# Kernel optimization log

Measured on AMD Instinct MI355X. Metric: run time of the kernel, lower is better.

Reference implementation:

```python
import jax, jax.numpy as jnp
import numpy as np

N_NODES = 50000
N_EDGES = 800000


def graph_conv(h, W, b, src, dst, n_nodes):
    # DGL GraphConv with norm='both':
    #   out = D_in^{-1/2} * A^T * (D_out^{-1/2} * h) @ W + b
    ones = jnp.ones((src.shape[0],), dtype=h.dtype)
    deg_out = jax.ops.segment_sum(ones, src, num_segments=n_nodes)
    deg_in = jax.ops.segment_sum(ones, dst, num_segments=n_nodes)
    norm_src = jnp.clip(deg_out, 1.0) ** -0.5  # [N]
    norm_dst = jnp.clip(deg_in, 1.0) ** -0.5   # [N]
    msg = (h * norm_src[:, None])[src]          # [E, F] gather
    agg = jax.ops.segment_sum(msg, dst, num_segments=n_nodes)  # [N, F] scatter
    return (agg * norm_dst[:, None]) @ W + b


def setup_inputs() -> dict:
    key = jax.random.key(0)
    ks = jax.random.split(key, 5)
    h = jax.random.normal(ks[0], (N_NODES, 64), dtype=jnp.float32)
    src = jax.random.randint(ks[1], (N_EDGES,), 0, N_NODES, dtype=jnp.int32)
    dst = jax.random.randint(ks[2], (N_EDGES,), 0, N_NODES, dtype=jnp.int32)
    W1 = jax.random.normal(ks[3], (64, 128), dtype=jnp.float32) * (1.0 / np.sqrt(64))
    b1 = jnp.zeros((128,), dtype=jnp.float32)
    W2 = jax.random.normal(ks[4], (128, 64), dtype=jnp.float32) * (1.0 / np.sqrt(128))
    b2 = jnp.zeros((64,), dtype=jnp.float32)
    return {"h": h, "src": src, "dst": dst, "W1": W1, "b1": b1, "W2": W2, "b2": b2}


def reference(h, src, dst, W1, b1, W2, b2):
    n = h.shape[0]
    h1 = jax.nn.relu(graph_conv(h, W1, b1, src, dst, n))
    out = graph_conv(h1, W2, b2, src, dst, n)
    return out
```

## Files before the change

### kernel.cpp

```cpp
#include <hip/hip_runtime.h>


#define NBMAX 512
#define CAPLOG 12
#define CAP (1 << CAPLOG)
#define NB_BIN 256

typedef __attribute__((ext_vector_type(8))) short bf16x8;
typedef __attribute__((ext_vector_type(4))) float f32x4;

__device__ inline unsigned short f2bf(float f) {
    unsigned int u = __float_as_uint(f);
    unsigned int r = (u + 0x7FFFu + ((u >> 16) & 1u)) >> 16;
    return (unsigned short)r;
}
__device__ inline float bf2f_lo(unsigned int u) { return __uint_as_float(u << 16); }
__device__ inline float bf2f_hi(unsigned int u) { return __uint_as_float(u & 0xFFFF0000u); }

__global__ __launch_bounds__(256) void hist_edges(const int* __restrict__ src,
        const int* __restrict__ dst, int* __restrict__ hist, int n_edges, int nb,
        const float* __restrict__ W1, const float* __restrict__ W2,
        unsigned short* __restrict__ w1t_g, unsigned short* __restrict__ w2t_g) {
    if (blockIdx.x == gridDim.x - 1) {
        for (int i = threadIdx.x; i < 8192; i += 256) {
            int k = i >> 7, nn = i & 127;
            w1t_g[nn * 72 + k] = f2bf(W1[i]);
        }
        for (int i = threadIdx.x; i < 8192; i += 256) {
            int k = i >> 6, nn = i & 63;
            w2t_g[nn * 136 + k] = f2bf(W2[i]);
        }
        return;
    }
    __shared__ int hs[NBMAX], hd[NBMAX];
    for (int i = threadIdx.x; i < nb; i += 256) { hs[i] = 0; hd[i] = 0; }
    __syncthreads();
    int chunk = (n_edges + NB_BIN - 1) / NB_BIN;
    int e0 = blockIdx.x * chunk;
    int e1 = e0 + chunk; if (e1 > n_edges) e1 = n_edges;
    for (int e = e0 + (int)threadIdx.x; e < e1; e += 256) {
        atomicAdd(&hs[src[e] >> 7], 1);
        atomicAdd(&hd[dst[e] >> 7], 1);
    }
    __syncthreads();
    int* rs = hist + (size_t)blockIdx.x * NBMAX;
    int* rd = hist + (size_t)(NB_BIN + blockIdx.x) * NBMAX;
    for (int i = threadIdx.x; i < nb; i += 256) { rs[i] = hs[i]; rd[i] = hd[i]; }
}

__global__ __launch_bounds__(256) void scan_hist(const int* __restrict__ hist,
        int* __restrict__ offs, int* __restrict__ cnt_s, int* __restrict__ cnt_d,
        int nb) {
    __shared__ int wtot[4];
    int j = blockIdx.x;
    int side = j >= nb ? 1 : 0;
    int bucket = j - side * nb;
    const int tid = threadIdx.x;
    size_t idx = (size_t)(side * NB_BIN + tid) * NBMAX + bucket;
    int v = hist[idx];
    int lane = tid & 63, wid = tid >> 6;
    int incl = v;
    #pragma unroll
    for (int d = 1; d < 64; d <<= 1) {
        int t = __shfl_up(incl, d, 64);
        if (lane >= d) incl += t;
    }
    if (lane == 63) wtot[wid] = incl;
    __syncthreads();
    int pre = 0;
    #pragma unroll
    for (int k = 0; k < 3; ++k) if (k < wid) pre += wtot[k];
    int excl = pre + incl - v;
    offs[idx] = excl;
    if (tid == 255) {
        int tot = excl + v;
        if (side) cnt_d[bucket] = tot; else cnt_s[bucket] = tot;
    }
}

__global__ __launch_bounds__(256) void scatter_binned(const int* __restrict__ src,
        const int* __restrict__ dst, const int* __restrict__ offs,
        unsigned char* __restrict__ ss, unsigned int* __restrict__ sd,
        int n_edges, int nb) {
    __shared__ int cs[NBMAX], cd[NBMAX];
    for (int i = threadIdx.x; i < nb; i += 256) {
        cs[i] = offs[(size_t)blockIdx.x * NBMAX + i];
        cd[i] = offs[(size_t)(NB_BIN + blockIdx.x) * NBMAX + i];
    }
    __syncthreads();
    int chunk = (n_edges + NB_BIN - 1) / NB_BIN;
    int e0 = blockIdx.x * chunk;
    int e1 = e0 + chunk; if (e1 > n_edges) e1 = n_edges;
    for (int e = e0 + (int)threadIdx.x; e < e1; e += 256) {
        int s = src[e], d = dst[e];
        int sb = s >> 7, db = d >> 7;
        int ps = atomicAdd(&cs[sb], 1);
        ss[((size_t)sb << CAPLOG) + ps] = (unsigned char)(s & 127);
        int pd = atomicAdd(&cd[db], 1);
        sd[((size_t)db << CAPLOG) + pd] = ((unsigned int)(d & 127) << 25) | (unsigned int)s;
    }
}

__global__ __launch_bounds__(256) void prep(const float* __restrict__ h,
        const unsigned char* __restrict__ ss, const int* __restrict__ cnt_s,
        const unsigned int* __restrict__ sd, const int* __restrict__ cnt_d,
        float* __restrict__ norm_src, unsigned short* __restrict__ xb,
        int2* __restrict__ node_rng, unsigned short* __restrict__ srt,
        float* __restrict__ norm_dst, int n) {
    __shared__ int cnt[128], cur[128];
    __shared__ float nrm[128];
    __shared__ int w0tot;
    const int b = blockIdx.x;
    const int tid = threadIdx.x;

    if (tid < 128) cnt[tid] = 0;
    __syncthreads();
    {
        int used = cnt_s[b];
        const unsigned char* p = ss + ((size_t)b << CAPLOG);
        for (int i = tid; i < used; i += 256) atomicAdd(&cnt[p[i]], 1);
    }
    __syncthreads();
    if (tid < 128) {
        int c = cnt[tid]; if (c < 1) c = 1;
        float s = 1.0f / sqrtf((float)c);
        nrm[tid] = s;
        int node = (b << 7) + tid;
        if (node < n) norm_src[node] = s;
    }
    __syncthreads();
    {
        int base = b << 7;
        for (int t = tid; t < 128 * 16; t += 256) {
            int r = t >> 4, c4 = (t & 15) << 2;
            int node = base + r;
            if (node < n) {
                float s = nrm[r];
                float4 v = *(const float4*)(h + (size_t)node * 64 + c4);
                ushort4 o;
                o.x = f2bf(v.x * s); o.y = f2bf(v.y * s);
                o.z = f2bf(v.z * s); o.w = f2bf(v.w * s);
                *(ushort4*)(xb + (size_t)node * 64 + c4) = o;
            }
        }
    }
    __syncthreads();

    if (tid < 128) cnt[tid] = 0;
    __syncthreads();
    int used = cnt_d[b];
    const unsigned int* p = sd + ((size_t)b << CAPLOG);
    for (int i = tid; i < used; i += 256) atomicAdd(&cnt[p[i] >> 25], 1);
    __syncthreads();
    int lane = tid & 63, wid = tid >> 6;
    int v = (tid < 128) ? cnt[tid] : 0;
    int incl = v;
    #pragma unroll
    for (int d = 1; d < 64; d <<= 1) {
        int t = __shfl_up(incl, d, 64);
        if (lane >= d) incl += t;
    }
    if (tid == 63) w0tot = incl;
    __syncthreads();
    if (tid < 128) {
        int excl = incl - v + (wid == 1 ? w0tot : 0);
        cur[tid] = excl;
        int node = (b << 7) + tid;
        if (node < n) {
            int base = b << CAPLOG;
            node_rng[node] = make_int2(base + excl, base + excl + v);
            int c = v; if (c < 1) c = 1;
            norm_dst[node] = 1.0f / sqrtf((float)c);
        }
    }
    __syncthreads();
    for (int i = tid; i < used; i += 256) {
        unsigned int e = p[i];
        int l = (int)(e >> 25);
        int pos = atomicAdd(&cur[l], 1);
        srt[((size_t)b << CAPLOG) + pos] = (unsigned short)(e & 0xFFFFu);
    }
}

__global__ __launch_bounds__(256) void gather24(const unsigned short* __restrict__ xb,
        const unsigned short* __restrict__ srt, const int2* __restrict__ node_rng,
        const float* __restrict__ nrm, const float* __restrict__ bias,
        void* __restrict__ outp, int write_bf, int n_nodes) {
    int node = blockIdx.x * 4 + (threadIdx.x >> 6);
    if (node >= n_nodes) return;
    int lane = threadIdx.x & 63;
    int g  = lane >> 3;
    int c8 = (lane & 7) * 8;
    int2 rng = node_rng[node];
    int a0 = rng.x, a1 = rng.y;
    float acc[8];
    #pragma unroll
    for (int j = 0; j < 8; ++j) acc[j] = 0.f;
    for (int base = a0; base < a1; base += 24) {
        #pragma unroll
        for (int u = 0; u < 3; ++u) {
            int ei = base + u * 8 + g;
            int idx = ei < a1 ? ei : a1 - 1;
            float msk = ei < a1 ? 1.0f : 0.0f;
            int s = srt[idx];
            const uint4 v = *(const uint4*)(xb + (size_t)s * 64 + c8);
            acc[0] = fmaf(bf2f_lo(v.x), msk, acc[0]);
            acc[1] = fmaf(bf2f_hi(v.x), msk, acc[1]);
            acc[2] = fmaf(bf2f_lo(v.y), msk, acc[2]);
            acc[3] = fmaf(bf2f_hi(v.y), msk, acc[3]);
            acc[4] = fmaf(bf2f_lo(v.z), msk, acc[4]);
            acc[5] = fmaf(bf2f_hi(v.z), msk, acc[5]);
            acc[6] = fmaf(bf2f_lo(v.w), msk, acc[6]);
            acc[7] = fmaf(bf2f_hi(v.w), msk, acc[7]);
        }
    }
    #pragma unroll
    for (int off = 8; off < 64; off <<= 1) {
        #pragma unroll
        for (int j = 0; j < 8; ++j) acc[j] += __shfl_xor(acc[j], off, 64);
    }
    if (g == 0) {
        float s = nrm[node];
        float r[8];
        #pragma unroll
        for (int j = 0; j < 8; ++j) r[j] = acc[j] * s;
        if (write_bf) {
            unsigned short rb[8];
            #pragma unroll
            for (int j = 0; j < 8; ++j) rb[j] = f2bf(r[j]);
            unsigned short* o = (unsigned short*)outp + (size_t)node * 64 + c8;
            *(ushort4*)(o)     = make_ushort4(rb[0], rb[1], rb[2], rb[3]);
            *(ushort4*)(o + 4) = make_ushort4(rb[4], rb[5], rb[6], rb[7]);
        } else {
            if (bias) {
                #pragma unroll
                for (int j = 0; j < 8; ++j) r[j] += bias[c8 + j];
            }
            float* o = (float*)outp + (size_t)node * 64 + c8;
            *(float4*)(o)     = make_float4(r[0], r[1], r[2], r[3]);
            *(float4*)(o + 4) = make_float4(r[4], r[5], r[6], r[7]);
        }
    }
}

__global__ __launch_bounds__(256) void gemm12(const unsigned short* __restrict__ Ab,
        const unsigned short* __restrict__ w1t_g, const float* __restrict__ b1,
        const float* __restrict__ norm, const unsigned short* __restrict__ w2t_g,
        unsigned short* __restrict__ y2b, int n) {
    __shared__ __align__(16) unsigned short W1t[128 * 72];
    __shared__ __align__(16) unsigned short W2t[64 * 136];
    __shared__ __align__(16) unsigned short Hs[64 * 136];
    __shared__ float b1s[128];
    const int tid = threadIdx.x;

    {
        const uint4* s1 = (const uint4*)w1t_g;
        uint4* d1 = (uint4*)W1t;
        for (int i = tid; i < 1152; i += 256) d1[i] = s1[i];
        const uint4* s2 = (const uint4*)w2t_g;
        uint4* d2 = (uint4*)W2t;
        for (int i = tid; i < 1088; i += 256) d2[i] = s2[i];
    }
    if (tid < 128) b1s[tid] = b1[tid];
    __syncthreads();

    const int w  = tid >> 6;
    const int l  = tid & 63;
    const int ln = l & 15;
    const int q  = l >> 4;
    const int m0 = blockIdx.x * 64 + w * 16;

    int arow = m0 + ln; if (arow > n - 1) arow = n - 1;
    const unsigned short* arp = Ab + (size_t)arow * 64 + q * 8;
    bf16x8 a0 = *(const bf16x8*)(arp);
    bf16x8 a1 = *(const bf16x8*)(arp + 32);

    float ns[4];
    #pragma unroll
    for (int r = 0; r < 4; ++r) {
        int node = m0 + q * 4 + r;
        ns[r] = norm[node < n ? node : n - 1];
    }

    #pragma unroll
    for (int c = 0; c < 8; ++c) {
        const unsigned short* bp = W1t + (c * 16 + ln) * 72 + q * 8;
        bf16x8 b0 = *(const bf16x8*)(bp);
        bf16x8 bk = *(const bf16x8*)(bp + 32);
        f32x4 acc = {0.f, 0.f, 0.f, 0.f};
        acc = __builtin_amdgcn_mfma_f32_16x16x32_bf16(a0, b0, acc, 0, 0, 0);
        acc = __builtin_amdgcn_mfma_f32_16x16x32_bf16(a1, bk, acc, 0, 0, 0);
        int col = c * 16 + ln;
        float bb = b1s[col];
        #pragma unroll
        for (int r = 0; r < 4; ++r) {
            float v = acc[r] + bb;
            v = v > 0.f ? v : 0.f;
            Hs[(w * 16 + q * 4 + r) * 136 + col] = f2bf(v * ns[r]);
        }
    }
    __syncthreads();

    const unsigned short* hp = Hs + (size_t)(w * 16 + ln) * 136 + q * 8;
    bf16x8 h0 = *(const bf16x8*)(hp);
    bf16x8 h1 = *(const bf16x8*)(hp + 32);
    bf16x8 h2 = *(const bf16x8*)(hp + 64);
    bf16x8 h3 = *(const bf16x8*)(hp + 96);
    #pragma unroll
    for (int c = 0; c < 4; ++c) {
        const unsigned short* bp = W2t + (c * 16 + ln) * 136 + q * 8;
        f32x4 acc = {0.f, 0.f, 0.f, 0.f};
        acc = __builtin_amdgcn_mfma_f32_16x16x32_bf16(h0, *(const bf16x8*)(bp),      acc, 0, 0, 0);
        acc = __builtin_amdgcn_mfma_f32_16x16x32_bf16(h1, *(const bf16x8*)(bp + 32), acc, 0, 0, 0);
        acc = __builtin_amdgcn_mfma_f32_16x16x32_bf16(h2, *(const bf16x8*)(bp + 64), acc, 0, 0, 0);
        acc = __builtin_amdgcn_mfma_f32_16x16x32_bf16(h3, *(const bf16x8*)(bp + 96), acc, 0, 0, 0);
        #pragma unroll
        for (int r = 0; r < 4; ++r) {
            int node = m0 + q * 4 + r;
            if (node < n)
                y2b[(size_t)node * 64 + c * 16 + ln] = f2bf(acc[r]);
        }
    }
}

extern "C" void kernel_launch(void* const* d_in, const int* in_sizes, int n_in,
                              void* d_out, int out_size, void* d_ws, size_t ws_size,
                              hipStream_t stream) {
    const float* h   = (const float*)d_in[0];
    const int*   src = (const int*)d_in[1];
    const int*   dst = (const int*)d_in[2];
    const float* W1  = (const float*)d_in[3];
    const float* b1  = (const float*)d_in[4];
    const float* W2  = (const float*)d_in[5];
    const float* b2  = (const float*)d_in[6];
    float* out = (float*)d_out;

    const int n = in_sizes[0] / 64;
    const int E = in_sizes[1];
    const int nb = (n + 127) >> 7;

    char* p = (char*)d_ws;
    auto alloc = [&](size_t bytes) {
        void* r = (void*)p;
        p += (bytes + 255) & ~(size_t)255;
        return r;
    };
    float* norm_src      = (float*)alloc((size_t)n * 4);
    float* norm_dst      = (float*)alloc((size_t)n * 4);
    int2* node_rng       = (int2*)alloc((size_t)n * 8);
    int* cnt_s           = (int*)alloc((size_t)nb * 4);
    int* cnt_d           = (int*)alloc((size_t)nb * 4);
    int* hist            = (int*)alloc((size_t)2 * NB_BIN * NBMAX * 4);
    int* offs            = (int*)alloc((size_t)2 * NB_BIN * NBMAX * 4);
    unsigned int* sd     = (unsigned int*)alloc((size_t)nb * CAP * 4);
    unsigned short* xb   = (unsigned short*)alloc((size_t)n * 64 * 2);
    unsigned short* agg1b= (unsigned short*)alloc((size_t)n * 64 * 2);
    unsigned short* y2b  = (unsigned short*)alloc((size_t)n * 64 * 2);
    unsigned short* srt  = (unsigned short*)alloc((size_t)nb * CAP * 2);
    unsigned char* ssb   = (unsigned char*)alloc((size_t)nb * CAP);
    unsigned short* w1t_g= (unsigned short*)alloc((size_t)128 * 72 * 2);
    unsigned short* w2t_g= (unsigned short*)alloc((size_t)64 * 136 * 2);

    hist_edges<<<NB_BIN + 1, 256, 0, stream>>>(src, dst, hist, E, nb,
                                               W1, W2, w1t_g, w2t_g);
    scan_hist<<<2 * nb, 256, 0, stream>>>(hist, offs, cnt_s, cnt_d, nb);
    scatter_binned<<<NB_BIN, 256, 0, stream>>>(src, dst, offs, ssb, sd, E, nb);
    prep<<<nb, 256, 0, stream>>>(h, ssb, cnt_s, sd, cnt_d, norm_src, xb,
                                 node_rng, srt, norm_dst, n);

    int gb = (n + 3) / 4;
    gather24<<<gb, 256, 0, stream>>>(xb, srt, node_rng, norm_dst, nullptr,
                                     (void*)agg1b, 1, n);

    int tb = (n + 63) / 64;
    gemm12<<<tb, 256, 0, stream>>>(agg1b, w1t_g, b1, norm_src, w2t_g, y2b, n);

    gather24<<<gb, 256, 0, stream>>>(y2b, srt, node_rng, norm_dst, b2,
                                     (void*)out, 0, n);
}
```

Before: 173.3 us.

## Split gathers into two source-half phases and widen edge binning grid

```diff
diff --git a/kernel.cpp b/kernel.cpp
--- a/kernel.cpp
+++ b/kernel.cpp
@@ -4,7 +4,7 @@
 #define NBMAX 512
 #define CAPLOG 12
 #define CAP (1 << CAPLOG)
-#define NB_BIN 256
+#define NBLK 1024
 
 typedef __attribute__((ext_vector_type(8))) short bf16x8;
 typedef __attribute__((ext_vector_type(4))) float f32x4;
@@ -21,7 +21,7 @@
         const int* __restrict__ dst, int* __restrict__ hist, int n_edges, int nb,
         const float* __restrict__ W1, const float* __restrict__ W2,
         unsigned short* __restrict__ w1t_g, unsigned short* __restrict__ w2t_g) {
-    if (blockIdx.x == gridDim.x - 1) {
+    if (blockIdx.x == NBLK) {
         for (int i = threadIdx.x; i < 8192; i += 256) {
             int k = i >> 7, nn = i & 127;
             w1t_g[nn * 72 + k] = f2bf(W1[i]);
@@ -35,7 +35,7 @@
     __shared__ int hs[NBMAX], hd[NBMAX];
     for (int i = threadIdx.x; i < nb; i += 256) { hs[i] = 0; hd[i] = 0; }
     __syncthreads();
-    int chunk = (n_edges + NB_BIN - 1) / NB_BIN;
+    int chunk = (n_edges + NBLK - 1) / NBLK;
     int e0 = blockIdx.x * chunk;
     int e1 = e0 + chunk; if (e1 > n_edges) e1 = n_edges;
     for (int e = e0 + (int)threadIdx.x; e < e1; e += 256) {
@@ -44,7 +44,7 @@
     }
     __syncthreads();
     int* rs = hist + (size_t)blockIdx.x * NBMAX;
-    int* rd = hist + (size_t)(NB_BIN + blockIdx.x) * NBMAX;
+    int* rd = hist + (size_t)(NBLK + blockIdx.x) * NBMAX;
     for (int i = threadIdx.x; i < nb; i += 256) { rs[i] = hs[i]; rd[i] = hd[i]; }
 }
 
@@ -56,10 +56,14 @@
     int side = j >= nb ? 1 : 0;
     int bucket = j - side * nb;
     const int tid = threadIdx.x;
-    size_t idx = (size_t)(side * NB_BIN + tid) * NBMAX + bucket;
-    int v = hist[idx];
+    size_t b0 = (size_t)(side * NBLK + tid * 4) * NBMAX + bucket;
+    int v0 = hist[b0];
+    int v1 = hist[b0 + NBMAX];
+    int v2 = hist[b0 + 2 * NBMAX];
+    int v3 = hist[b0 + 3 * NBMAX];
+    int s = v0 + v1 + v2 + v3;
     int lane = tid & 63, wid = tid >> 6;
-    int incl = v;
+    int incl = s;
     #pragma unroll
     for (int d = 1; d < 64; d <<= 1) {
         int t = __shfl_up(incl, d, 64);
@@ -70,10 +74,13 @@
     int pre = 0;
     #pragma unroll
     for (int k = 0; k < 3; ++k) if (k < wid) pre += wtot[k];
-    int excl = pre + incl - v;
-    offs[idx] = excl;
+    int eb = pre + incl - s;
+    offs[b0]             = eb;
+    offs[b0 + NBMAX]     = eb + v0;
+    offs[b0 + 2 * NBMAX] = eb + v0 + v1;
+    offs[b0 + 3 * NBMAX] = eb + v0 + v1 + v2;
     if (tid == 255) {
-        int tot = excl + v;
+        int tot = eb + s;
         if (side) cnt_d[bucket] = tot; else cnt_s[bucket] = tot;
     }
 }
@@ -85,10 +92,10 @@
     __shared__ int cs[NBMAX], cd[NBMAX];
     for (int i = threadIdx.x; i < nb; i += 256) {
         cs[i] = offs[(size_t)blockIdx.x * NBMAX + i];
-        cd[i] = offs[(size_t)(NB_BIN + blockIdx.x) * NBMAX + i];
-    }
-    __syncthreads();
-    int chunk = (n_edges + NB_BIN - 1) / NB_BIN;
+        cd[i] = offs[(size_t)(NBLK + blockIdx.x) * NBMAX + i];
+    }
+    __syncthreads();
+    int chunk = (n_edges + NBLK - 1) / NBLK;
     int e0 = blockIdx.x * chunk;
     int e1 = e0 + chunk; if (e1 > n_edges) e1 = n_edges;
     for (int e = e0 + (int)threadIdx.x; e < e1; e += 256) {
@@ -101,15 +108,14 @@
     }
 }
 
-__global__ __launch_bounds__(256) void prep(const float* __restrict__ h,
+__global__ __launch_bounds__(256) void prep_a(
         const unsigned char* __restrict__ ss, const int* __restrict__ cnt_s,
         const unsigned int* __restrict__ sd, const int* __restrict__ cnt_d,
-        float* __restrict__ norm_src, unsigned short* __restrict__ xb,
-        int2* __restrict__ node_rng, unsigned short* __restrict__ srt,
-        float* __restrict__ norm_dst, int n) {
-    __shared__ int cnt[128], cur[128];
-    __shared__ float nrm[128];
-    __shared__ int w0tot;
+        float* __restrict__ norm_src, int4* __restrict__ node_rng4,
+        unsigned short* __restrict__ srt, float* __restrict__ norm_dst,
+        int n, int nhalf) {
+    __shared__ int cnt[256], cur[256];
+    __shared__ int wtot[4];
     const int b = blockIdx.x;
     const int tid = threadIdx.x;
 
@@ -123,79 +129,95 @@
     __syncthreads();
     if (tid < 128) {
         int c = cnt[tid]; if (c < 1) c = 1;
-        float s = 1.0f / sqrtf((float)c);
-        nrm[tid] = s;
         int node = (b << 7) + tid;
-        if (node < n) norm_src[node] = s;
-    }
-    __syncthreads();
-    {
-        int base = b << 7;
-        for (int t = tid; t < 128 * 16; t += 256) {
-            int r = t >> 4, c4 = (t & 15) << 2;
-            int node = base + r;
-            if (node < n) {
-                float s = nrm[r];
-                float4 v = *(const float4*)(h + (size_t)node * 64 + c4);
-                ushort4 o;
-                o.x = f2bf(v.x * s); o.y = f2bf(v.y * s);
-                o.z = f2bf(v.z * s); o.w = f2bf(v.w * s);
-                *(ushort4*)(xb + (size_t)node * 64 + c4) = o;
-            }
-        }
-    }
-    __syncthreads();
-
-    if (tid < 128) cnt[tid] = 0;
+        if (node < n) norm_src[node] = 1.0f / sqrtf((float)c);
+    }
+    __syncthreads();
+
+    cnt[tid] = 0;
     __syncthreads();
     int used = cnt_d[b];
     const unsigned int* p = sd + ((size_t)b << CAPLOG);
-    for (int i = tid; i < used; i += 256) atomicAdd(&cnt[p[i] >> 25], 1);
+    for (int i = tid; i < used; i += 256) {
+        unsigned int e = p[i];
+        int key = ((int)(e >> 25) << 1) | ((int)(e & 0x1FFFFFFu) >= nhalf ? 1 : 0);
+        atomicAdd(&cnt[key], 1);
+    }
     __syncthreads();
     int lane = tid & 63, wid = tid >> 6;
-    int v = (tid < 128) ? cnt[tid] : 0;
+    int v = cnt[tid];
     int incl = v;
     #pragma unroll
     for (int d = 1; d < 64; d <<= 1) {
         int t = __shfl_up(incl, d, 64);
         if (lane >= d) incl += t;
     }
-    if (tid == 63) w0tot = incl;
+    if (lane == 63) wtot[wid] = incl;
+    __syncthreads();
+    int pre = 0;
+    #pragma unroll
+    for (int k = 0; k < 3; ++k) if (k < wid) pre += wtot[k];
+    cur[tid] = pre + incl - v;
     __syncthreads();
     if (tid < 128) {
-        int excl = incl - v + (wid == 1 ? w0tot : 0);
-        cur[tid] = excl;
+        int start = cur[2 * tid];
+        int mid   = cur[2 * tid + 1];
+        int end   = mid + cnt[2 * tid + 1];
         int node = (b << 7) + tid;
         if (node < n) {
             int base = b << CAPLOG;
-            node_rng[node] = make_int2(base + excl, base + excl + v);
-            int c = v; if (c < 1) c = 1;
+            node_rng4[node] = make_int4(base + start, base + mid, base + end, 0);
+            int c = end - start; if (c < 1) c = 1;
             norm_dst[node] = 1.0f / sqrtf((float)c);
         }
     }
     __syncthreads();
     for (int i = tid; i < used; i += 256) {
         unsigned int e = p[i];
-        int l = (int)(e >> 25);
-        int pos = atomicAdd(&cur[l], 1);
-        srt[((size_t)b << CAPLOG) + pos] = (unsigned short)(e & 0xFFFFu);
-    }
-}
-
-__global__ __launch_bounds__(256) void gather24(const unsigned short* __restrict__ xb,
-        const unsigned short* __restrict__ srt, const int2* __restrict__ node_rng,
+        int s = (int)(e & 0x1FFFFFFu);
+        int key = ((int)(e >> 25) << 1) | (s >= nhalf ? 1 : 0);
+        int pos = atomicAdd(&cur[key], 1);
+        srt[((size_t)b << CAPLOG) + pos] = (unsigned short)(s & 0xFFFF);
+    }
+}
+
+__global__ __launch_bounds__(256) void xcast(const float* __restrict__ h,
+        const float* __restrict__ norm_src, unsigned short* __restrict__ xb,
+        int n) {
+    int idx = blockIdx.x * 256 + threadIdx.x;
+    if (idx >= n * 16) return;
+    int node = idx >> 4, c4 = (idx & 15) << 2;
+    float s = norm_src[node];
+    float4 v = *(const float4*)(h + (size_t)node * 64 + c4);
+    ushort4 o;
+    o.x = f2bf(v.x * s); o.y = f2bf(v.y * s);
+    o.z = f2bf(v.z * s); o.w = f2bf(v.w * s);
+    *(ushort4*)(xb + (size_t)node * 64 + c4) = o;
+}
+
+__global__ __launch_bounds__(256) void gather_ph(const unsigned short* __restrict__ xb,
+        const unsigned short* __restrict__ srt, const int4* __restrict__ node_rng4,
         const float* __restrict__ nrm, const float* __restrict__ bias,
-        void* __restrict__ outp, int write_bf, int n_nodes) {
+        float* __restrict__ accbuf, void* __restrict__ outp,
+        int write_bf, int phase, int n_nodes) {
     int node = blockIdx.x * 4 + (threadIdx.x >> 6);
     if (node >= n_nodes) return;
     int lane = threadIdx.x & 63;
     int g  = lane >> 3;
     int c8 = (lane & 7) * 8;
-    int2 rng = node_rng[node];
-    int a0 = rng.x, a1 = rng.y;
+    int4 rng = node_rng4[node];
+    int a0 = phase ? rng.y : rng.x;
+    int a1 = phase ? rng.z : rng.y;
+    f32x4* ap = (f32x4*)(accbuf + (size_t)node * 64 + c8);
     float acc[8];
     #pragma unroll
     for (int j = 0; j < 8; ++j) acc[j] = 0.f;
+    if (phase && g == 0) {
+        f32x4 p0 = __builtin_nontemporal_load(ap);
+        f32x4 p1 = __builtin_nontemporal_load(ap + 1);
+        acc[0] = p0.x; acc[1] = p0.y; acc[2] = p0.z; acc[3] = p0.w;
+        acc[4] = p1.x; acc[5] = p1.y; acc[6] = p1.z; acc[7] = p1.w;
+    }
     for (int base = a0; base < a1; base += 24) {
         #pragma unroll
         for (int u = 0; u < 3; ++u) {
@@ -220,25 +242,32 @@
         for (int j = 0; j < 8; ++j) acc[j] += __shfl_xor(acc[j], off, 64);
     }
     if (g == 0) {
-        float s = nrm[node];
-        float r[8];
-        #pragma unroll
-        for (int j = 0; j < 8; ++j) r[j] = acc[j] * s;
-        if (write_bf) {
-            unsigned short rb[8];
+        if (!phase) {
+            f32x4 q0; q0.x = acc[0]; q0.y = acc[1]; q0.z = acc[2]; q0.w = acc[3];
+            f32x4 q1; q1.x = acc[4]; q1.y = acc[5]; q1.z = acc[6]; q1.w = acc[7];
+            __builtin_nontemporal_store(q0, ap);
+            __builtin_nontemporal_store(q1, ap + 1);
+        } else {
+            float s = nrm[node];
+            float r[8];
             #pragma unroll
-            for (int j = 0; j < 8; ++j) rb[j] = f2bf(r[j]);
-            unsigned short* o = (unsigned short*)outp + (size_t)node * 64 + c8;
-            *(ushort4*)(o)     = make_ushort4(rb[0], rb[1], rb[2], rb[3]);
-            *(ushort4*)(o + 4) = make_ushort4(rb[4], rb[5], rb[6], rb[7]);
-        } else {
-            if (bias) {
+            for (int j = 0; j < 8; ++j) r[j] = acc[j] * s;
+            if (write_bf) {
+                unsigned short rb[8];
                 #pragma unroll
-                for (int j = 0; j < 8; ++j) r[j] += bias[c8 + j];
+                for (int j = 0; j < 8; ++j) rb[j] = f2bf(r[j]);
+                unsigned short* o = (unsigned short*)outp + (size_t)node * 64 + c8;
+                *(ushort4*)(o)     = make_ushort4(rb[0], rb[1], rb[2], rb[3]);
+                *(ushort4*)(o + 4) = make_ushort4(rb[4], rb[5], rb[6], rb[7]);
+            } else {
+                if (bias) {
+                    #pragma unroll
+                    for (int j = 0; j < 8; ++j) r[j] += bias[c8 + j];
+                }
+                float* o = (float*)outp + (size_t)node * 64 + c8;
+                *(float4*)(o)     = make_float4(r[0], r[1], r[2], r[3]);
+                *(float4*)(o + 4) = make_float4(r[4], r[5], r[6], r[7]);
             }
-            float* o = (float*)outp + (size_t)node * 64 + c8;
-            *(float4*)(o)     = make_float4(r[0], r[1], r[2], r[3]);
-            *(float4*)(o + 4) = make_float4(r[4], r[5], r[6], r[7]);
         }
     }
 }
@@ -338,6 +367,7 @@
     const int n = in_sizes[0] / 64;
     const int E = in_sizes[1];
     const int nb = (n + 127) >> 7;
+    const int nhalf = n >> 1;
 
     char* p = (char*)d_ws;
     auto alloc = [&](size_t bytes) {
@@ -347,12 +377,13 @@
     };
     float* norm_src      = (float*)alloc((size_t)n * 4);
     float* norm_dst      = (float*)alloc((size_t)n * 4);
-    int2* node_rng       = (int2*)alloc((size_t)n * 8);
+    int4* node_rng4      = (int4*)alloc((size_t)n * 16);
     int* cnt_s           = (int*)alloc((size_t)nb * 4);
     int* cnt_d           = (int*)alloc((size_t)nb * 4);
-    int* hist            = (int*)alloc((size_t)2 * NB_BIN * NBMAX * 4);
-    int* offs            = (int*)alloc((size_t)2 * NB_BIN * NBMAX * 4);
+    int* hist            = (int*)alloc((size_t)2 * NBLK * NBMAX * 4);
+    int* offs            = (int*)alloc((size_t)2 * NBLK * NBMAX * 4);
     unsigned int* sd     = (unsigned int*)alloc((size_t)nb * CAP * 4);
+    float* accbuf        = (float*)alloc((size_t)n * 64 * 4);
     unsigned short* xb   = (unsigned short*)alloc((size_t)n * 64 * 2);
     unsigned short* agg1b= (unsigned short*)alloc((size_t)n * 64 * 2);
     unsigned short* y2b  = (unsigned short*)alloc((size_t)n * 64 * 2);
@@ -361,20 +392,25 @@
     unsigned short* w1t_g= (unsigned short*)alloc((size_t)128 * 72 * 2);
     unsigned short* w2t_g= (unsigned short*)alloc((size_t)64 * 136 * 2);
 
-    hist_edges<<<NB_BIN + 1, 256, 0, stream>>>(src, dst, hist, E, nb,
-                                               W1, W2, w1t_g, w2t_g);
+    hist_edges<<<NBLK + 1, 256, 0, stream>>>(src, dst, hist, E, nb,
+                                             W1, W2, w1t_g, w2t_g);
     scan_hist<<<2 * nb, 256, 0, stream>>>(hist, offs, cnt_s, cnt_d, nb);
-    scatter_binned<<<NB_BIN, 256, 0, stream>>>(src, dst, offs, ssb, sd, E, nb);
-    prep<<<nb, 256, 0, stream>>>(h, ssb, cnt_s, sd, cnt_d, norm_src, xb,
-                                 node_rng, srt, norm_dst, n);
+    scatter_binned<<<NBLK, 256, 0, stream>>>(src, dst, offs, ssb, sd, E, nb);
+    prep_a<<<nb, 256, 0, stream>>>(ssb, cnt_s, sd, cnt_d, norm_src,
+                                   node_rng4, srt, norm_dst, n, nhalf);
+    xcast<<<(n * 16 + 255) / 256, 256, 0, stream>>>(h, norm_src, xb, n);
 
     int gb = (n + 3) / 4;
-    gather24<<<gb, 256, 0, stream>>>(xb, srt, node_rng, norm_dst, nullptr,
-                                     (void*)agg1b, 1, n);
+    gather_ph<<<gb, 256, 0, stream>>>(xb, srt, node_rng4, norm_dst, nullptr,
+                                      accbuf, (void*)agg1b, 1, 0, n);
+    gather_ph<<<gb, 256, 0, stream>>>(xb, srt, node_rng4, norm_dst, nullptr,
+                                      accbuf, (void*)agg1b, 1, 1, n);
 
     int tb = (n + 63) / 64;
     gemm12<<<tb, 256, 0, stream>>>(agg1b, w1t_g, b1, norm_src, w2t_g, y2b, n);
 
-    gather24<<<gb, 256, 0, stream>>>(y2b, srt, node_rng, norm_dst, b2,
-                                     (void*)out, 0, n);
-}
+    gather_ph<<<gb, 256, 0, stream>>>(y2b, srt, node_rng4, norm_dst, b2,
+                                      accbuf, (void*)out, 0, 0, n);
+    gather_ph<<<gb, 256, 0, stream>>>(y2b, srt, node_rng4, norm_dst, b2,
+                                      accbuf, (void*)out, 0, 1, n);
+}
```

Result: slower. 222.3 us (+28.2%).
